# Performance work log

Measured on AMD Instinct MI355X. Metric: run time of the kernel, lower is better.

Reference implementation:

```python
import jax, jax.numpy as jnp
import numpy as np

EPS = float(np.finfo(np.float32).eps)


def setup_inputs() -> dict:
    key = jax.random.key(0)
    k1, k2, k3 = jax.random.split(key, 3)
    T, D, E = 8192, 2048, 64
    x = jax.random.normal(k1, (T, D), dtype=jnp.float32)
    wg_weight = jax.random.normal(k2, (E, D), dtype=jnp.float32) * 0.02
    u = jax.random.uniform(k3, (T, E), dtype=jnp.float32, minval=1e-6, maxval=1.0 - 1e-6)
    gumbel_noise = -jnp.log(-jnp.log(u))  # standard Gumbel(0,1) rsample
    return {"x": x, "wg_weight": wg_weight, "gumbel_noise": gumbel_noise}


def reference(x, wg_weight, gumbel_noise):
    # logits = wg(input): [T, E]
    logits = x @ wg_weight.T
    T, E = logits.shape
    capacity = 2 * ((T + E - 1) // E)  # training mode: 2 * ceil(T/E)

    gates = jax.nn.softmax(logits, axis=1)

    # top-1 expert
    idx1 = jnp.argmax(gates, axis=1)                       # [T]
    mask1 = jax.nn.one_hot(idx1, E, dtype=jnp.float32)     # [T, E]

    # second expert via gumbel-noised logits, masking out expert 1
    logits_w_noise = logits + gumbel_noise
    logits_except1 = jnp.where(mask1 > 0, -jnp.inf, logits_w_noise)
    idx2 = jnp.argmax(logits_except1, axis=1)
    mask2 = jax.nn.one_hot(idx2, E, dtype=jnp.float32)

    # capacity assignment: position of each token in its expert's queue
    locations1 = jnp.cumsum(mask1, axis=0) - 1.0           # [T, E]
    locations2 = jnp.cumsum(mask2, axis=0) - 1.0 + jnp.sum(mask1, axis=0, keepdims=True)

    # aux load-balancing loss
    me = jnp.mean(gates, axis=0)
    ce = jnp.mean(mask1, axis=0)
    l_aux = jnp.mean(me * ce) * E * E

    # drop tokens over capacity
    mask1 = mask1 * (locations1 < capacity)
    mask2 = mask2 * (locations2 < capacity)

    # gate values, renormalized over the two (kept) experts
    gates1_s = jnp.sum(gates * mask1, axis=1)
    gates2_s = jnp.sum(gates * mask2, axis=1)
    denom = jnp.maximum(gates1_s + gates2_s, EPS)
    gates1_s = gates1_s / denom
    gates2_s = gates2_s / denom

    # capacity slot index per token (0 for dropped tokens)
    loc1_s = jnp.sum(locations1 * mask1, axis=1).astype(jnp.int32)   # [T]
    loc2_s = jnp.sum(locations2 * mask2, axis=1).astype(jnp.int32)
    loc1_sc = jax.nn.one_hot(loc1_s, capacity, dtype=jnp.float32)    # [T, C]
    loc2_sc = jax.nn.one_hot(loc2_s, capacity, dtype=jnp.float32)

    # combine_weights[t, e, c] = gate_s[t] * mask[t, e] * onehot_loc[t, c]
    combine1 = jnp.einsum('t,te,tc->tec', gates1_s, mask1, loc1_sc)
    combine2 = jnp.einsum('t,te,tc->tec', gates2_s, mask2, loc2_sc)
    combine_weights = combine1 + combine2                   # [T, E, C]
    dispatch_mask = combine_weights.astype(bool)

    return l_aux, combine_weights, dispatch_mask
```

## Files before the change

### kernel.cpp

```cpp
#include <hip/hip_runtime.h>
#include <math.h>

#define T_TOK 8192
#define D_DIM 2048
#define E_EXP 64
#define CAP   256
#define NCHUNK 32
#define TEC   (134217728LL)
#define TE    (T_TOK * E_EXP)
#define KSPLIT 4
#define KLEN   (D_DIM / KSPLIT)

__device__ __forceinline__ int swz(int r) { return (r & 7) ^ ((r >> 3) & 7); }

__global__ __launch_bounds__(256) void k_gemm(const float* __restrict__ x,
                                              const float* __restrict__ wg,
                                              float* __restrict__ part) {
  __shared__ float xs[32 * 64];
  __shared__ float ws[64 * 64];
  const int tid = threadIdx.x;
  const int row0 = (blockIdx.x >> 2) * 32;
  const int kc = blockIdx.x & 3;
  const int kbase = kc * KLEN;
  const int rr = tid >> 4;
  const int cc = tid & 15;
  const int sA0 = swz(rr), sA1 = swz(rr + 16);
  const int sB0 = swz(cc * 4 + 0), sB1 = swz(cc * 4 + 1);
  const int sB2 = swz(cc * 4 + 2), sB3 = swz(cc * 4 + 3);
  float acc[2][4] = {{0.f, 0.f, 0.f, 0.f}, {0.f, 0.f, 0.f, 0.f}};
  for (int k0 = kbase; k0 < kbase + KLEN; k0 += 64) {
#pragma unroll
    for (int i = 0; i < 2; ++i) {
      const int f = tid + i * 256;
      const int r = f >> 4, g = f & 15;
      const float4 v = *reinterpret_cast<const float4*>(
          &x[(size_t)(row0 + r) * D_DIM + k0 + g * 4]);
      *reinterpret_cast<float4*>(&xs[r * 64 + ((g ^ swz(r)) << 2)]) = v;
    }
#pragma unroll
    for (int i = 0; i < 4; ++i) {
      const int f = tid + i * 256;
      const int r = f >> 4, g = f & 15;
      const float4 v = *reinterpret_cast<const float4*>(
          &wg[(size_t)r * D_DIM + k0 + g * 4]);
      *reinterpret_cast<float4*>(&ws[r * 64 + ((g ^ swz(r)) << 2)]) = v;
    }
    __syncthreads();
#pragma unroll
    for (int g = 0; g < 16; ++g) {
      const float4 a0 = *reinterpret_cast<const float4*>(&xs[rr * 64 + ((g ^ sA0) << 2)]);
      const float4 a1 = *reinterpret_cast<const float4*>(&xs[(rr + 16) * 64 + ((g ^ sA1) << 2)]);
      const float4 b0 = *reinterpret_cast<const float4*>(&ws[(cc * 4 + 0) * 64 + ((g ^ sB0) << 2)]);
      const float4 b1 = *reinterpret_cast<const float4*>(&ws[(cc * 4 + 1) * 64 + ((g ^ sB1) << 2)]);
      const float4 b2 = *reinterpret_cast<const float4*>(&ws[(cc * 4 + 2) * 64 + ((g ^ sB2) << 2)]);
      const float4 b3 = *reinterpret_cast<const float4*>(&ws[(cc * 4 + 3) * 64 + ((g ^ sB3) << 2)]);
      acc[0][0] = fmaf(a0.x, b0.x, acc[0][0]); acc[0][0] = fmaf(a0.y, b0.y, acc[0][0]);
      acc[0][0] = fmaf(a0.z, b0.z, acc[0][0]); acc[0][0] = fmaf(a0.w, b0.w, acc[0][0]);
      acc[0][1] = fmaf(a0.x, b1.x, acc[0][1]); acc[0][1] = fmaf(a0.y, b1.y, acc[0][1]);
      acc[0][1] = fmaf(a0.z, b1.z, acc[0][1]); acc[0][1] = fmaf(a0.w, b1.w, acc[0][1]);
      acc[0][2] = fmaf(a0.x, b2.x, acc[0][2]); acc[0][2] = fmaf(a0.y, b2.y, acc[0][2]);
      acc[0][2] = fmaf(a0.z, b2.z, acc[0][2]); acc[0][2] = fmaf(a0.w, b2.w, acc[0][2]);
      acc[0][3] = fmaf(a0.x, b3.x, acc[0][3]); acc[0][3] = fmaf(a0.y, b3.y, acc[0][3]);
      acc[0][3] = fmaf(a0.z, b3.z, acc[0][3]); acc[0][3] = fmaf(a0.w, b3.w, acc[0][3]);
      acc[1][0] = fmaf(a1.x, b0.x, acc[1][0]); acc[1][0] = fmaf(a1.y, b0.y, acc[1][0]);
      acc[1][0] = fmaf(a1.z, b0.z, acc[1][0]); acc[1][0] = fmaf(a1.w, b0.w, acc[1][0]);
      acc[1][1] = fmaf(a1.x, b1.x, acc[1][1]); acc[1][1] = fmaf(a1.y, b1.y, acc[1][1]);
      acc[1][1] = fmaf(a1.z, b1.z, acc[1][1]); acc[1][1] = fmaf(a1.w, b1.w, acc[1][1]);
      acc[1][2] = fmaf(a1.x, b2.x, acc[1][2]); acc[1][2] = fmaf(a1.y, b2.y, acc[1][2]);
      acc[1][2] = fmaf(a1.z, b2.z, acc[1][2]); acc[1][2] = fmaf(a1.w, b2.w, acc[1][2]);
      acc[1][3] = fmaf(a1.x, b3.x, acc[1][3]); acc[1][3] = fmaf(a1.y, b3.y, acc[1][3]);
      acc[1][3] = fmaf(a1.z, b3.z, acc[1][3]); acc[1][3] = fmaf(a1.w, b3.w, acc[1][3]);
    }
    __syncthreads();
  }
  const float4 o0 = make_float4(acc[0][0], acc[0][1], acc[0][2], acc[0][3]);
  const float4 o1 = make_float4(acc[1][0], acc[1][1], acc[1][2], acc[1][3]);
  float* pbase = part + (size_t)kc * TE;
  *reinterpret_cast<float4*>(&pbase[(size_t)(row0 + rr) * E_EXP + cc * 4]) = o0;
  *reinterpret_cast<float4*>(&pbase[(size_t)(row0 + rr + 16) * E_EXP + cc * 4]) = o1;
}

__global__ __launch_bounds__(256) void k_gate(const float* __restrict__ part,
                                              const float* __restrict__ gumbel,
                                              float* __restrict__ colpart,
                                              int* __restrict__ idx1,
                                              int* __restrict__ idx2,
                                              float* __restrict__ g1v,
                                              float* __restrict__ g2v) {
  const int lane = threadIdx.x & 63;
  const int wave = threadIdx.x >> 6;
  const int gwave = blockIdx.x * 4 + wave;
  float colacc = 0.f;
  for (int i = 0; i < 8; ++i) {
    const int t = gwave + i * 1024;
    const int o = t * 64 + lane;
    const float L = (part[o] + part[TE + o]) + (part[2 * TE + o] + part[3 * TE + o]);
    float m = L;
#pragma unroll
    for (int off = 32; off; off >>= 1) m = fmaxf(m, __shfl_xor(m, off));
    const float e = expf(L - m);
    float s = e;
#pragma unroll
    for (int off = 32; off; off >>= 1) s += __shfl_xor(s, off);
    const float g = e / s;
    colacc += g;
    float v = g; int ix = lane;
#pragma unroll
    for (int off = 32; off; off >>= 1) {
      float v2 = __shfl_xor(v, off); int i2 = __shfl_xor(ix, off);
      if (v2 > v || (v2 == v && i2 < ix)) { v = v2; ix = i2; }
    }
    const int i1 = ix;
    const float gate1 = __shfl(g, i1);
    float nz = L + gumbel[o];
    if (lane == i1) nz = -INFINITY;
    float v2v = nz; int ix2 = lane;
#pragma unroll
    for (int off = 32; off; off >>= 1) {
      float v2 = __shfl_xor(v2v, off); int j2 = __shfl_xor(ix2, off);
      if (v2 > v2v || (v2 == v2v && j2 < ix2)) { v2v = v2; ix2 = j2; }
    }
    const int i2x = ix2;
    const float gate2 = __shfl(g, i2x);
    if (lane == 0) { idx1[t] = i1; idx2[t] = i2x; g1v[t] = gate1; g2v[t] = gate2; }
  }
  __shared__ float cs[4][64];
  cs[wave][lane] = colacc;
  __syncthreads();
  if (wave == 0) {
    float ssum = cs[0][lane] + cs[1][lane] + cs[2][lane] + cs[3][lane];
    colpart[blockIdx.x * 64 + lane] = ssum;
  }
}

__global__ __launch_bounds__(256) void k_rank(const int* __restrict__ idx1,
                                              const int* __restrict__ idx2,
                                              int* __restrict__ rank1,
                                              int* __restrict__ rank2,
                                              int* __restrict__ hist1,
                                              int* __restrict__ hist2) {
  __shared__ int s1[256], s2[256];
  __shared__ int h1[64], h2[64];
  const int tid = threadIdx.x;
  const int base = blockIdx.x * 256;
  if (tid < 64) { h1[tid] = 0; h2[tid] = 0; }
  s1[tid] = idx1[base + tid];
  s2[tid] = idx2[base + tid];
  __syncthreads();
  const int my1 = s1[tid], my2 = s2[tid];
  int r1 = 0, r2 = 0;
  for (int j = 0; j < 256; ++j) {
    r1 += (j < tid && s1[j] == my1);
    r2 += (j < tid && s2[j] == my2);
  }
  atomicAdd(&h1[my1], 1);
  atomicAdd(&h2[my2], 1);
  rank1[base + tid] = r1;
  rank2[base + tid] = r2;
  __syncthreads();
  if (tid < 64) {
    hist1[blockIdx.x * 64 + tid] = h1[tid];
    hist2[blockIdx.x * 64 + tid] = h2[tid];
  }
}

__global__ __launch_bounds__(64) void k_prefix(const int* __restrict__ hist1,
                                               const int* __restrict__ hist2,
                                               const float* __restrict__ colpart,
                                               int* __restrict__ offs1,
                                               int* __restrict__ offs2,
                                               float* __restrict__ dout) {
  const int e = threadIdx.x;
  int run = 0;
  for (int c = 0; c < NCHUNK; ++c) { offs1[c * 64 + e] = run; run += hist1[c * 64 + e]; }
  const int total1 = run;
  int run2 = total1;
  for (int c = 0; c < NCHUNK; ++c) { offs2[c * 64 + e] = run2; run2 += hist2[c * 64 + e]; }
  float csum = 0.f;
  for (int b = 0; b < 256; ++b) csum += colpart[b * 64 + e];
  const float me = csum / (float)T_TOK;
  const float ce = (float)total1 / (float)T_TOK;
  float val = me * ce;
#pragma unroll
  for (int o = 32; o; o >>= 1) val += __shfl_xor(val, o);
  if (e == 0) dout[0] = val * (float)E_EXP;
}

__global__ __launch_bounds__(256) void k_scatter(const int* __restrict__ idx1,
                                                 const int* __restrict__ idx2,
                                                 const float* __restrict__ g1v,
                                                 const float* __restrict__ g2v,
                                                 const int* __restrict__ rank1,
                                                 const int* __restrict__ rank2,
                                                 const int* __restrict__ offs1,
                                                 const int* __restrict__ offs2,
                                                 float* __restrict__ dout) {
  const int t = blockIdx.x * 256 + threadIdx.x;
  const int c = t >> 8;
  const int e1 = idx1[t], e2 = idx2[t];
  const int loc1 = offs1[c * 64 + e1] + rank1[t];
  const int loc2 = offs2[c * 64 + e2] + rank2[t];
  const bool k1 = loc1 < CAP;
  const bool k2 = loc2 < CAP;
  const float a = k1 ? g1v[t] : 0.f;
  const float b = k2 ? g2v[t] : 0.f;
  const float denom = fmaxf(a + b, 1.1920929e-7f);
  if (k1) {
    const long long o = 1LL + ((long long)t * 64 + e1) * 256 + loc1;
    dout[o] = a / denom;
    dout[o + TEC] = 1.0f;
  }
  if (k2) {
    const long long o = 1LL + ((long long)t * 64 + e2) * 256 + loc2;
    dout[o] = b / denom;
    dout[o + TEC] = 1.0f;
  }
}

extern "C" void kernel_launch(void* const* d_in, const int* in_sizes, int n_in,
                              void* d_out, int out_size, void* d_ws, size_t ws_size,
                              hipStream_t stream) {
  const float* x = (const float*)d_in[0];
  const float* wg = (const float*)d_in[1];
  const float* gumbel = (const float*)d_in[2];
  float* dout = (float*)d_out;

  char* p = (char*)d_ws;
  float* part = (float*)p;              p += (size_t)KSPLIT * TE * 4;
  float* colpart = (float*)p;           p += 256 * 64 * 4;
  float* g1v = (float*)p;               p += T_TOK * 4;
  float* g2v = (float*)p;               p += T_TOK * 4;
  int* idx1 = (int*)p;                  p += T_TOK * 4;
  int* idx2 = (int*)p;                  p += T_TOK * 4;
  int* rank1 = (int*)p;                 p += T_TOK * 4;
  int* rank2 = (int*)p;                 p += T_TOK * 4;
  int* hist1 = (int*)p;                 p += NCHUNK * 64 * 4;
  int* hist2 = (int*)p;                 p += NCHUNK * 64 * 4;
  int* offs1 = (int*)p;                 p += NCHUNK * 64 * 4;
  int* offs2 = (int*)p;                 p += NCHUNK * 64 * 4;

  hipMemsetAsync(d_out, 0, (size_t)out_size * sizeof(float), stream);

  k_gemm<<<(T_TOK / 32) * KSPLIT, 256, 0, stream>>>(x, wg, part);
  k_gate<<<256, 256, 0, stream>>>(part, gumbel, colpart, idx1, idx2, g1v, g2v);
  k_rank<<<NCHUNK, 256, 0, stream>>>(idx1, idx2, rank1, rank2, hist1, hist2);
  k_prefix<<<1, 64, 0, stream>>>(hist1, hist2, colpart, offs1, offs2, dout);
  k_scatter<<<NCHUNK, 256, 0, stream>>>(idx1, idx2, g1v, g2v, rank1, rank2,
                                        offs1, offs2, dout);
}
```

Baseline: 263.1 us.

## Replace output memset plus sparse scatter with one dense writer kernel

Drops the full-output hipMemsetAsync and the sparse scatter kernel. A new kernel writes every element of the combine-weights and dispatch-mask tensors once with float4 stores, placing the few nonzero values inline. Because the output is offset by one float (l_aux at index 0), the float4 stores are misaligned relative to logical rows, so lane 0 recomputes boundary values from the previous token. This removes one full pass over roughly a gigabyte of output but adds per-element branching and redundant index loads.

```diff
diff --git a/kernel.cpp b/kernel.cpp
--- a/kernel.cpp
+++ b/kernel.cpp
@@ -10,6 +10,7 @@
 #define TE    (T_TOK * E_EXP)
 #define KSPLIT 4
 #define KLEN   (D_DIM / KSPLIT)
+#define EPSV   1.1920929e-7f
 
 __device__ __forceinline__ int swz(int r) { return (r & 7) ^ ((r >> 3) & 7); }
 
@@ -169,6 +170,7 @@
                                                const float* __restrict__ colpart,
                                                int* __restrict__ offs1,
                                                int* __restrict__ offs2,
+                                               float* __restrict__ lauxw,
                                                float* __restrict__ dout) {
   const int e = threadIdx.x;
   int run = 0;
@@ -183,37 +185,89 @@
   float val = me * ce;
 #pragma unroll
   for (int o = 32; o; o >>= 1) val += __shfl_xor(val, o);
-  if (e == 0) dout[0] = val * (float)E_EXP;
-}
-
-__global__ __launch_bounds__(256) void k_scatter(const int* __restrict__ idx1,
-                                                 const int* __restrict__ idx2,
-                                                 const float* __restrict__ g1v,
-                                                 const float* __restrict__ g2v,
-                                                 const int* __restrict__ rank1,
-                                                 const int* __restrict__ rank2,
-                                                 const int* __restrict__ offs1,
-                                                 const int* __restrict__ offs2,
-                                                 float* __restrict__ dout) {
-  const int t = blockIdx.x * 256 + threadIdx.x;
-  const int c = t >> 8;
-  const int e1 = idx1[t], e2 = idx2[t];
-  const int loc1 = offs1[c * 64 + e1] + rank1[t];
-  const int loc2 = offs2[c * 64 + e2] + rank2[t];
-  const bool k1 = loc1 < CAP;
-  const bool k2 = loc2 < CAP;
-  const float a = k1 ? g1v[t] : 0.f;
-  const float b = k2 ? g2v[t] : 0.f;
-  const float denom = fmaxf(a + b, 1.1920929e-7f);
-  if (k1) {
-    const long long o = 1LL + ((long long)t * 64 + e1) * 256 + loc1;
-    dout[o] = a / denom;
-    dout[o + TEC] = 1.0f;
-  }
-  if (k2) {
-    const long long o = 1LL + ((long long)t * 64 + e2) * 256 + loc2;
-    dout[o] = b / denom;
-    dout[o + TEC] = 1.0f;
+  if (e == 0) { const float la = val * (float)E_EXP; dout[0] = la; lauxw[0] = la; }
+}
+
+__global__ __launch_bounds__(256) void k_mat(const int* __restrict__ idx1,
+                                             const int* __restrict__ idx2,
+                                             const float* __restrict__ g1v,
+                                             const float* __restrict__ g2v,
+                                             const int* __restrict__ rank1,
+                                             const int* __restrict__ rank2,
+                                             const int* __restrict__ offs1,
+                                             const int* __restrict__ offs2,
+                                             const float* __restrict__ lauxw,
+                                             float* __restrict__ dout) {
+  const int lane = threadIdx.x & 63;
+  const int w = threadIdx.x >> 6;
+  const long long WS = (long long)blockIdx.x * 131072 + (long long)w * 32768;
+  const bool firstwave = (blockIdx.x == 0 && w == 0);
+  for (int tt = 0; tt < 2; ++tt) {
+    const long long base = WS + (long long)tt * 16384;
+    const bool half = base >= TEC;
+    const long long rbase = half ? (base - TEC) : base;
+    const int t = (int)(rbase >> 14);
+    const int e1 = idx1[t], e2 = idx2[t];
+    const int l1 = offs1[(t >> 8) * 64 + e1] + rank1[t];
+    const int l2 = offs2[(t >> 8) * 64 + e2] + rank2[t];
+    const bool k1 = l1 < CAP, k2 = l2 < CAP;
+    const float a = k1 ? g1v[t] : 0.f;
+    const float b = k2 ? g2v[t] : 0.f;
+    const float dn = fmaxf(a + b, EPSV);
+    const float w1v = half ? 1.f : a / dn;
+    const float w2v = half ? 1.f : b / dn;
+    float* po = dout + base + 4 * lane;
+    for (int i = 0; i < 64; ++i) {
+      float4 v = make_float4(0.f, 0.f, 0.f, 0.f);
+      const bool r1 = k1 && (e1 == i);
+      const bool r2 = k2 && (e2 == i);
+      if (lane == 0) {
+        if (firstwave && tt == 0 && i == 0) {
+          v.x = lauxw[0];
+        } else if (i == 0) {
+          const long long idxp = base - 1;
+          const bool hp = idxp >= TEC;
+          const long long rp = hp ? (idxp - TEC) : idxp;
+          const int tp = (int)(rp >> 14);
+          const int ep = (int)((rp >> 8) & 63);
+          const int e1p = idx1[tp], e2p = idx2[tp];
+          const int l1p = offs1[(tp >> 8) * 64 + e1p] + rank1[tp];
+          const int l2p = offs2[(tp >> 8) * 64 + e2p] + rank2[tp];
+          const bool k1p = l1p < CAP, k2p = l2p < CAP;
+          const float ap = k1p ? g1v[tp] : 0.f;
+          const float bp = k2p ? g2v[tp] : 0.f;
+          const float dp = fmaxf(ap + bp, EPSV);
+          float val = 0.f;
+          if (k1p && ep == e1p && l1p == 255) val = hp ? 1.f : ap / dp;
+          if (k2p && ep == e2p && l2p == 255) val = hp ? 1.f : bp / dp;
+          v.x = val;
+        } else {
+          const int ep = i - 1;
+          if (k1 && ep == e1 && l1 == 255) v.x = w1v;
+          if (k2 && ep == e2 && l2 == 255) v.x = w2v;
+        }
+      } else {
+        const int k = 4 * lane - 1;
+        if (r1 && k == l1) v.x = w1v;
+        if (r2 && k == l2) v.x = w2v;
+      }
+      if (r1) {
+        const int d = l1 - 4 * lane;
+        if (d == 0) v.y = w1v; else if (d == 1) v.z = w1v; else if (d == 2) v.w = w1v;
+      }
+      if (r2) {
+        const int d = l2 - 4 * lane;
+        if (d == 0) v.y = w2v; else if (d == 1) v.z = w2v; else if (d == 2) v.w = w2v;
+      }
+      *reinterpret_cast<float4*>(po) = v;
+      po += 256;
+    }
+    if (blockIdx.x == 2047 && w == 3 && tt == 1 && lane == 63) {
+      float val = 0.f;
+      if (k1 && e1 == 63 && l1 == 255) val = 1.f;
+      if (k2 && e2 == 63 && l2 == 255) val = 1.f;
+      dout[2LL * TEC] = val;
+    }
   }
 }
 
@@ -238,13 +292,12 @@
   int* hist2 = (int*)p;                 p += NCHUNK * 64 * 4;
   int* offs1 = (int*)p;                 p += NCHUNK * 64 * 4;
   int* offs2 = (int*)p;                 p += NCHUNK * 64 * 4;
-
-  hipMemsetAsync(d_out, 0, (size_t)out_size * sizeof(float), stream);
+  float* lauxw = (float*)p;             p += 64;
 
   k_gemm<<<(T_TOK / 32) * KSPLIT, 256, 0, stream>>>(x, wg, part);
   k_gate<<<256, 256, 0, stream>>>(part, gumbel, colpart, idx1, idx2, g1v, g2v);
   k_rank<<<NCHUNK, 256, 0, stream>>>(idx1, idx2, rank1, rank2, hist1, hist2);
-  k_prefix<<<1, 64, 0, stream>>>(hist1, hist2, colpart, offs1, offs2, dout);
-  k_scatter<<<NCHUNK, 256, 0, stream>>>(idx1, idx2, g1v, g2v, rank1, rank2,
-                                        offs1, offs2, dout);
-}
+  k_prefix<<<1, 64, 0, stream>>>(hist1, hist2, colpart, offs1, offs2, lauxw, dout);
+  k_mat<<<2048, 256, 0, stream>>>(idx1, idx2, g1v, g2v, rank1, rank2,
+                                  offs1, offs2, lauxw, dout);
+}
```

Result: slower. 282.4 us (+7.4%).

## Fuse rank, prefix and scatter kernels into one tail kernel with grid barrier

Applied to the files above, without the earlier changes.

Merges the per-chunk rank, single-block prefix sum and scatter kernels into one kernel. The last block to arrive, found through an atomic ticket, computes the offsets and the aux loss, then releases the others, which spin on a flag. Ranks stay in registers instead of going through global memory. This removes two kernel launches and the global round trips between them, but relies on all 32 blocks being resident at once and adds spin-wait and atomic overhead.

```diff
diff --git a/kernel.cpp b/kernel.cpp
--- a/kernel.cpp
+++ b/kernel.cpp
@@ -10,6 +10,7 @@
 #define TE    (T_TOK * E_EXP)
 #define KSPLIT 4
 #define KLEN   (D_DIM / KSPLIT)
+#define EPSV   1.1920929e-7f
 
 __device__ __forceinline__ int swz(int r) { return (r & 7) ^ ((r >> 3) & 7); }
 
@@ -86,7 +87,9 @@
                                               int* __restrict__ idx1,
                                               int* __restrict__ idx2,
                                               float* __restrict__ g1v,
-                                              float* __restrict__ g2v) {
+                                              float* __restrict__ g2v,
+                                              unsigned int* __restrict__ sync) {
+  if (blockIdx.x == 0 && threadIdx.x < 2) atomicExch(&sync[threadIdx.x], 0u);
   const int lane = threadIdx.x & 63;
   const int wave = threadIdx.x >> 6;
   const int gwave = blockIdx.x * 4 + wave;
@@ -133,16 +136,23 @@
   }
 }
 
-__global__ __launch_bounds__(256) void k_rank(const int* __restrict__ idx1,
+__global__ __launch_bounds__(256) void k_tail(const int* __restrict__ idx1,
                                               const int* __restrict__ idx2,
-                                              int* __restrict__ rank1,
-                                              int* __restrict__ rank2,
-                                              int* __restrict__ hist1,
-                                              int* __restrict__ hist2) {
+                                              const float* __restrict__ g1v,
+                                              const float* __restrict__ g2v,
+                                              const float* __restrict__ colpart,
+                                              int* __restrict__ histG1,
+                                              int* __restrict__ histG2,
+                                              int* __restrict__ offsG1,
+                                              int* __restrict__ offsG2,
+                                              unsigned int* __restrict__ sync,
+                                              float* __restrict__ dout) {
   __shared__ int s1[256], s2[256];
   __shared__ int h1[64], h2[64];
+  __shared__ int ticket_s;
   const int tid = threadIdx.x;
-  const int base = blockIdx.x * 256;
+  const int bid = blockIdx.x;
+  const int base = bid * 256;
   if (tid < 64) { h1[tid] = 0; h2[tid] = 0; }
   s1[tid] = idx1[base + tid];
   s2[tid] = idx2[base + tid];
@@ -155,63 +165,60 @@
   }
   atomicAdd(&h1[my1], 1);
   atomicAdd(&h2[my2], 1);
-  rank1[base + tid] = r1;
-  rank2[base + tid] = r2;
   __syncthreads();
   if (tid < 64) {
-    hist1[blockIdx.x * 64 + tid] = h1[tid];
-    hist2[blockIdx.x * 64 + tid] = h2[tid];
-  }
-}
-
-__global__ __launch_bounds__(64) void k_prefix(const int* __restrict__ hist1,
-                                               const int* __restrict__ hist2,
-                                               const float* __restrict__ colpart,
-                                               int* __restrict__ offs1,
-                                               int* __restrict__ offs2,
-                                               float* __restrict__ dout) {
-  const int e = threadIdx.x;
-  int run = 0;
-  for (int c = 0; c < NCHUNK; ++c) { offs1[c * 64 + e] = run; run += hist1[c * 64 + e]; }
-  const int total1 = run;
-  int run2 = total1;
-  for (int c = 0; c < NCHUNK; ++c) { offs2[c * 64 + e] = run2; run2 += hist2[c * 64 + e]; }
-  float csum = 0.f;
-  for (int b = 0; b < 256; ++b) csum += colpart[b * 64 + e];
-  const float me = csum / (float)T_TOK;
-  const float ce = (float)total1 / (float)T_TOK;
-  float val = me * ce;
-#pragma unroll
-  for (int o = 32; o; o >>= 1) val += __shfl_xor(val, o);
-  if (e == 0) dout[0] = val * (float)E_EXP;
-}
-
-__global__ __launch_bounds__(256) void k_scatter(const int* __restrict__ idx1,
-                                                 const int* __restrict__ idx2,
-                                                 const float* __restrict__ g1v,
-                                                 const float* __restrict__ g2v,
-                                                 const int* __restrict__ rank1,
-                                                 const int* __restrict__ rank2,
-                                                 const int* __restrict__ offs1,
-                                                 const int* __restrict__ offs2,
-                                                 float* __restrict__ dout) {
-  const int t = blockIdx.x * 256 + threadIdx.x;
-  const int c = t >> 8;
-  const int e1 = idx1[t], e2 = idx2[t];
-  const int loc1 = offs1[c * 64 + e1] + rank1[t];
-  const int loc2 = offs2[c * 64 + e2] + rank2[t];
+    atomicExch(&histG1[bid * 64 + tid], h1[tid]);
+    atomicExch(&histG2[bid * 64 + tid], h2[tid]);
+  }
+  __threadfence();
+  __syncthreads();
+  if (tid == 0) ticket_s = (int)atomicAdd(&sync[0], 1u);
+  __syncthreads();
+  if (ticket_s == NCHUNK - 1) {
+    if (tid < 64) {
+      const int e = tid;
+      int hh1[NCHUNK], hh2[NCHUNK];
+#pragma unroll
+      for (int c = 0; c < NCHUNK; ++c) hh1[c] = atomicAdd(&histG1[c * 64 + e], 0);
+#pragma unroll
+      for (int c = 0; c < NCHUNK; ++c) hh2[c] = atomicAdd(&histG2[c * 64 + e], 0);
+      int run = 0;
+#pragma unroll
+      for (int c = 0; c < NCHUNK; ++c) { atomicExch(&offsG1[c * 64 + e], run); run += hh1[c]; }
+      const int total1 = run;
+      int run2 = total1;
+#pragma unroll
+      for (int c = 0; c < NCHUNK; ++c) { atomicExch(&offsG2[c * 64 + e], run2); run2 += hh2[c]; }
+      float csum = 0.f;
+      for (int b = 0; b < 256; ++b) csum += colpart[b * 64 + e];
+      const float me = csum / (float)T_TOK;
+      const float ce = (float)total1 / (float)T_TOK;
+      float val = me * ce;
+#pragma unroll
+      for (int o = 32; o; o >>= 1) val += __shfl_xor(val, o);
+      if (e == 0) dout[0] = val * (float)E_EXP;
+    }
+    __threadfence();
+    __syncthreads();
+    if (tid == 0) atomicExch(&sync[1], 1u);
+  }
+  if (tid == 0) { while (atomicAdd(&sync[1], 0u) == 0u) { } }
+  __syncthreads();
+  const int t = base + tid;
+  const int loc1 = atomicAdd(&offsG1[bid * 64 + my1], 0) + r1;
+  const int loc2 = atomicAdd(&offsG2[bid * 64 + my2], 0) + r2;
   const bool k1 = loc1 < CAP;
   const bool k2 = loc2 < CAP;
   const float a = k1 ? g1v[t] : 0.f;
   const float b = k2 ? g2v[t] : 0.f;
-  const float denom = fmaxf(a + b, 1.1920929e-7f);
+  const float denom = fmaxf(a + b, EPSV);
   if (k1) {
-    const long long o = 1LL + ((long long)t * 64 + e1) * 256 + loc1;
+    const long long o = 1LL + ((long long)t * 64 + my1) * 256 + loc1;
     dout[o] = a / denom;
     dout[o + TEC] = 1.0f;
   }
   if (k2) {
-    const long long o = 1LL + ((long long)t * 64 + e2) * 256 + loc2;
+    const long long o = 1LL + ((long long)t * 64 + my2) * 256 + loc2;
     dout[o] = b / denom;
     dout[o + TEC] = 1.0f;
   }
@@ -232,19 +239,16 @@
   float* g2v = (float*)p;               p += T_TOK * 4;
   int* idx1 = (int*)p;                  p += T_TOK * 4;
   int* idx2 = (int*)p;                  p += T_TOK * 4;
-  int* rank1 = (int*)p;                 p += T_TOK * 4;
-  int* rank2 = (int*)p;                 p += T_TOK * 4;
-  int* hist1 = (int*)p;                 p += NCHUNK * 64 * 4;
-  int* hist2 = (int*)p;                 p += NCHUNK * 64 * 4;
-  int* offs1 = (int*)p;                 p += NCHUNK * 64 * 4;
-  int* offs2 = (int*)p;                 p += NCHUNK * 64 * 4;
+  int* histG1 = (int*)p;                p += NCHUNK * 64 * 4;
+  int* histG2 = (int*)p;                p += NCHUNK * 64 * 4;
+  int* offsG1 = (int*)p;                p += NCHUNK * 64 * 4;
+  int* offsG2 = (int*)p;                p += NCHUNK * 64 * 4;
+  unsigned int* sync = (unsigned int*)p; p += 256;
 
   hipMemsetAsync(d_out, 0, (size_t)out_size * sizeof(float), stream);
 
   k_gemm<<<(T_TOK / 32) * KSPLIT, 256, 0, stream>>>(x, wg, part);
-  k_gate<<<256, 256, 0, stream>>>(part, gumbel, colpart, idx1, idx2, g1v, g2v);
-  k_rank<<<NCHUNK, 256, 0, stream>>>(idx1, idx2, rank1, rank2, hist1, hist2);
-  k_prefix<<<1, 64, 0, stream>>>(hist1, hist2, colpart, offs1, offs2, dout);
-  k_scatter<<<NCHUNK, 256, 0, stream>>>(idx1, idx2, g1v, g2v, rank1, rank2,
-                                        offs1, offs2, dout);
-}
+  k_gate<<<256, 256, 0, stream>>>(part, gumbel, colpart, idx1, idx2, g1v, g2v, sync);
+  k_tail<<<NCHUNK, 256, 0, stream>>>(idx1, idx2, g1v, g2v, colpart,
+                                     histG1, histG2, offsG1, offsG2, sync, dout);
+}
```

After: 265.1 us. Within noise of the previous version (+0.8%).
